# Kernel optimization log

Hardware: AMD Instinct MI355X
Metric: run time of the kernel (lower is better)

## Reference

```python
import jax, jax.numpy as jnp
import numpy as np

NEG_INF = -1e30


def setup_inputs() -> dict:
    key = jax.random.key(0)
    k1, k2, k3 = jax.random.split(key, 3)
    B, L, D = 32, 4096, 1024
    sequence = jax.random.normal(k1, (B, L, D), dtype=jnp.float32)
    vector = jax.random.normal(k2, (B, D), dtype=jnp.float32)
    sequence_mask = jax.random.randint(k3, (B, L), 0, 2, dtype=jnp.int32)
    return {"sequence": sequence, "vector": vector, "sequence_mask": sequence_mask}


def reference(sequence, vector, sequence_mask):
    # DotProduct similarity: score[b,l] = <sequence[b,l,:], vector[b,:]>
    scores = jnp.einsum("bld,bd->bl", sequence, vector)
    mask = sequence_mask.astype(scores.dtype)
    # masked softmax over the sequence length dimension
    masked_scores = jnp.where(mask > 0, scores, NEG_INF)
    weights = jax.nn.softmax(masked_scores, axis=-1)
    # attention pooling: weighted sum of sequence positions -> [B, D]
    pooled = jnp.einsum("bl,bld->bd", weights, sequence)
    return pooled, weights
```

## Files before the change

### kernel.cpp

```cpp
#include <hip/hip_runtime.h>
#include <math.h>

constexpr int B = 32;
constexpr int L = 4096;
constexpr int D = 1024;
constexpr float NEG_INF = -1e30f;

constexpr int CH  = 128;
constexpr int RPW = L / CH;

using f32x4 = __attribute__((ext_vector_type(4))) float;

constexpr size_t WS_SCORES = 0;
constexpr size_t WS_PM     = WS_SCORES + (size_t)B * L;
constexpr size_t WS_PL     = WS_PM + (size_t)B * CH;
constexpr size_t WS_MDEN   = WS_PL + (size_t)B * CH;
constexpr size_t WS_PACC   = WS_MDEN + 2 * B;

__global__ __launch_bounds__(256, 4) void pass1_kernel(
    const float* __restrict__ seq, const float* __restrict__ vec,
    const int* __restrict__ mask, float* __restrict__ scores,
    float* __restrict__ pm, float* __restrict__ pl, float* __restrict__ pacc)
{
    const int wave = blockIdx.x * 4 + (threadIdx.x >> 6);
    const int lane = threadIdx.x & 63;
    const int b = wave >> 7;
    const int c = wave & (CH - 1);
    const int l0 = c * RPW;

    const f32x4* v4 = (const f32x4*)(vec + (size_t)b * D);
    const f32x4 v0 = v4[lane], v1 = v4[lane + 64], v2 = v4[lane + 128], v3 = v4[lane + 192];

    float m = -INFINITY, lsum = 0.f;
    f32x4 a0 = {0,0,0,0}, a1 = {0,0,0,0}, a2 = {0,0,0,0}, a3 = {0,0,0,0};

    const f32x4* srow = (const f32x4*)(seq + ((size_t)b * L + l0) * D);
    const int rowbase = b * L + l0;

    for (int it = 0; it < RPW / 2; ++it) {
        const int2 mk = *(const int2*)(mask + rowbase + it * 2);

        const f32x4* p0 = srow + (size_t)(it * 2) * (D / 4);
        const f32x4* p1 = p0 + (D / 4);
        f32x4 s00 = __builtin_nontemporal_load(p0 + lane);
        f32x4 s01 = __builtin_nontemporal_load(p0 + lane + 64);
        f32x4 s02 = __builtin_nontemporal_load(p0 + lane + 128);
        f32x4 s03 = __builtin_nontemporal_load(p0 + lane + 192);
        f32x4 s10 = __builtin_nontemporal_load(p1 + lane);
        f32x4 s11 = __builtin_nontemporal_load(p1 + lane + 64);
        f32x4 s12 = __builtin_nontemporal_load(p1 + lane + 128);
        f32x4 s13 = __builtin_nontemporal_load(p1 + lane + 192);

        f32x4 d0v = s00 * v0 + s01 * v1 + s02 * v2 + s03 * v3;
        f32x4 d1v = s10 * v0 + s11 * v1 + s12 * v2 + s13 * v3;
        float dot0 = d0v.x + d0v.y + d0v.z + d0v.w;
        float dot1 = d1v.x + d1v.y + d1v.z + d1v.w;

        #pragma unroll
        for (int off = 32; off; off >>= 1) {
            dot0 += __shfl_xor(dot0, off, 64);
            dot1 += __shfl_xor(dot1, off, 64);
        }

        const float sc0 = (mk.x > 0) ? dot0 : NEG_INF;
        const float sc1 = (mk.y > 0) ? dot1 : NEG_INF;

        if (sc0 > m) {
            const float scale = __expf(m - sc0);
            lsum *= scale;
            a0 *= scale; a1 *= scale; a2 *= scale; a3 *= scale;
            m = sc0;
        }
        {
            const float p = __expf(sc0 - m);
            lsum += p;
            a0 += p * s00; a1 += p * s01; a2 += p * s02; a3 += p * s03;
        }
        if (sc1 > m) {
            const float scale = __expf(m - sc1);
            lsum *= scale;
            a0 *= scale; a1 *= scale; a2 *= scale; a3 *= scale;
            m = sc1;
        }
        {
            const float p = __expf(sc1 - m);
            lsum += p;
            a0 += p * s10; a1 += p * s11; a2 += p * s12; a3 += p * s13;
        }

        if (lane == 0) *(float2*)(scores + rowbase + it * 2) = make_float2(sc0, sc1);
    }

    f32x4* aout = (f32x4*)(pacc + (size_t)wave * D);
    aout[lane] = a0; aout[lane + 64] = a1; aout[lane + 128] = a2; aout[lane + 192] = a3;
    if (lane == 0) { pm[wave] = m; pl[wave] = lsum; }
}

__global__ __launch_bounds__(128) void combine_kernel(
    const float* __restrict__ pm, const float* __restrict__ pl,
    const float* __restrict__ pacc, float* __restrict__ pooled,
    float* __restrict__ Mden)
{
    const int b  = blockIdx.x;
    const int ds = blockIdx.y * 128;
    const int t  = threadIdx.x;

    __shared__ float red[128];
    __shared__ float wgt[128];

    const float mc = pm[b * CH + t];
    const float lc = pl[b * CH + t];

    red[t] = mc; __syncthreads();
    #pragma unroll
    for (int s = 64; s; s >>= 1) { if (t < s) red[t] = fmaxf(red[t], red[t + s]); __syncthreads(); }
    const float M = red[0];
    __syncthreads();

    const float e = __expf(mc - M);
    wgt[t] = e;
    red[t] = lc * e; __syncthreads();
    #pragma unroll
    for (int s = 64; s; s >>= 1) { if (t < s) red[t] += red[t + s]; __syncthreads(); }
    const float denom = red[0];
    const float inv = 1.f / denom;

    float acc = 0.f;
    const float* base = pacc + (size_t)b * CH * D + ds + t;
    #pragma unroll 8
    for (int c = 0; c < CH; ++c)
        acc += base[(size_t)c * D] * wgt[c];

    pooled[b * D + ds + t] = acc * inv;
    if (blockIdx.y == 0 && t == 0) { Mden[2*b] = M; Mden[2*b + 1] = denom; }
}

__global__ __launch_bounds__(256) void weights_kernel(
    const float* __restrict__ scores, const float* __restrict__ Mden,
    float* __restrict__ out_w)
{
    const int idx = blockIdx.x * 256 + threadIdx.x;
    const int b = idx >> 12;
    const float M   = Mden[2*b];
    const float den = Mden[2*b + 1];
    out_w[idx] = __expf(scores[idx] - M) / den;
}

extern "C" void kernel_launch(void* const* d_in, const int* in_sizes, int n_in,
                              void* d_out, int out_size, void* d_ws, size_t ws_size,
                              hipStream_t stream) {
    const float* seq  = (const float*)d_in[0];
    const float* vec  = (const float*)d_in[1];
    const int*   mask = (const int*)d_in[2];
    float* out = (float*)d_out;

    float* ws     = (float*)d_ws;
    float* scores = ws + WS_SCORES;
    float* pm     = ws + WS_PM;
    float* pl     = ws + WS_PL;
    float* Mden   = ws + WS_MDEN;
    float* pacc   = ws + WS_PACC;

    pass1_kernel<<<(B * CH) / 4, 256, 0, stream>>>(seq, vec, mask, scores, pm, pl, pacc);
    combine_kernel<<<dim3(B, D / 128), 128, 0, stream>>>(pm, pl, pacc, out, Mden);
    weights_kernel<<<(B * L) / 256, 256, 0, stream>>>(scores, Mden, out + B * D);
}
```

Before: 667.6 us.

## Fuse weights normalization into combine kernel and batch online-softmax rescale per pair

The separate weights kernel is removed. Each combine block, which already knows the row max and denominator, now normalizes a 512-element slice of scores with vectorized loads and stores. This saves one kernel launch and the Mden round trip. In pass1, the online-softmax rescale now happens once per pair of rows using the max of both scores instead of once per row, which cuts exp calls and branches. The combine loop unroll also goes from 8 to 16.

```diff
diff --git a/kernel.cpp b/kernel.cpp
--- a/kernel.cpp
+++ b/kernel.cpp
@@ -14,8 +14,8 @@
 constexpr size_t WS_SCORES = 0;
 constexpr size_t WS_PM     = WS_SCORES + (size_t)B * L;
 constexpr size_t WS_PL     = WS_PM + (size_t)B * CH;
-constexpr size_t WS_MDEN   = WS_PL + (size_t)B * CH;
-constexpr size_t WS_PACC   = WS_MDEN + 2 * B;
+constexpr size_t WS_PAD    = WS_PL + (size_t)B * CH;
+constexpr size_t WS_PACC   = WS_PAD + 2 * B;
 
 __global__ __launch_bounds__(256, 4) void pass1_kernel(
     const float* __restrict__ seq, const float* __restrict__ vec,
@@ -65,28 +65,18 @@
         const float sc0 = (mk.x > 0) ? dot0 : NEG_INF;
         const float sc1 = (mk.y > 0) ? dot1 : NEG_INF;
 
-        if (sc0 > m) {
-            const float scale = __expf(m - sc0);
+        const float mNew = fmaxf(fmaxf(sc0, sc1), m);
+        if (mNew > m) {
+            const float scale = __expf(m - mNew);
             lsum *= scale;
             a0 *= scale; a1 *= scale; a2 *= scale; a3 *= scale;
-            m = sc0;
+            m = mNew;
         }
-        {
-            const float p = __expf(sc0 - m);
-            lsum += p;
-            a0 += p * s00; a1 += p * s01; a2 += p * s02; a3 += p * s03;
-        }
-        if (sc1 > m) {
-            const float scale = __expf(m - sc1);
-            lsum *= scale;
-            a0 *= scale; a1 *= scale; a2 *= scale; a3 *= scale;
-            m = sc1;
-        }
-        {
-            const float p = __expf(sc1 - m);
-            lsum += p;
-            a0 += p * s10; a1 += p * s11; a2 += p * s12; a3 += p * s13;
-        }
+        const float p0w = __expf(sc0 - m);
+        const float p1w = __expf(sc1 - m);
+        lsum += p0w + p1w;
+        a0 += p0w * s00; a1 += p0w * s01; a2 += p0w * s02; a3 += p0w * s03;
+        a0 += p1w * s10; a1 += p1w * s11; a2 += p1w * s12; a3 += p1w * s13;
 
         if (lane == 0) *(float2*)(scores + rowbase + it * 2) = make_float2(sc0, sc1);
     }
@@ -98,11 +88,12 @@
 
 __global__ __launch_bounds__(128) void combine_kernel(
     const float* __restrict__ pm, const float* __restrict__ pl,
-    const float* __restrict__ pacc, float* __restrict__ pooled,
-    float* __restrict__ Mden)
+    const float* __restrict__ pacc, const float* __restrict__ scores,
+    float* __restrict__ pooled, float* __restrict__ out_w)
 {
     const int b  = blockIdx.x;
-    const int ds = blockIdx.y * 128;
+    const int y  = blockIdx.y;
+    const int ds = y * 128;
     const int t  = threadIdx.x;
 
     __shared__ float red[128];
@@ -127,23 +118,19 @@
 
     float acc = 0.f;
     const float* base = pacc + (size_t)b * CH * D + ds + t;
-    #pragma unroll 8
+    #pragma unroll 16
     for (int c = 0; c < CH; ++c)
         acc += base[(size_t)c * D] * wgt[c];
+    pooled[b * D + ds + t] = acc * inv;
 
-    pooled[b * D + ds + t] = acc * inv;
-    if (blockIdx.y == 0 && t == 0) { Mden[2*b] = M; Mden[2*b + 1] = denom; }
-}
-
-__global__ __launch_bounds__(256) void weights_kernel(
-    const float* __restrict__ scores, const float* __restrict__ Mden,
-    float* __restrict__ out_w)
-{
-    const int idx = blockIdx.x * 256 + threadIdx.x;
-    const int b = idx >> 12;
-    const float M   = Mden[2*b];
-    const float den = Mden[2*b + 1];
-    out_w[idx] = __expf(scores[idx] - M) / den;
+    const int l0 = y * 512;
+    const f32x4 s4 = ((const f32x4*)(scores + (size_t)b * L + l0))[t];
+    f32x4 w;
+    w.x = __expf(s4.x - M) * inv;
+    w.y = __expf(s4.y - M) * inv;
+    w.z = __expf(s4.z - M) * inv;
+    w.w = __expf(s4.w - M) * inv;
+    ((f32x4*)(out_w + (size_t)b * L + l0))[t] = w;
 }
 
 extern "C" void kernel_launch(void* const* d_in, const int* in_sizes, int n_in,
@@ -158,10 +145,8 @@
     float* scores = ws + WS_SCORES;
     float* pm     = ws + WS_PM;
     float* pl     = ws + WS_PL;
-    float* Mden   = ws + WS_MDEN;
     float* pacc   = ws + WS_PACC;
 
     pass1_kernel<<<(B * CH) / 4, 256, 0, stream>>>(seq, vec, mask, scores, pm, pl, pacc);
-    combine_kernel<<<dim3(B, D / 128), 128, 0, stream>>>(pm, pl, pacc, out, Mden);
-    weights_kernel<<<(B * L) / 256, 256, 0, stream>>>(scores, Mden, out + B * D);
+    combine_kernel<<<dim3(B, D / 128), 128, 0, stream>>>(pm, pl, pacc, scores, out, out + B * D);
 }
```

After: 664.7 us. Within noise of the previous version (-0.4%).
